# Performance work log

Measured on AMD Instinct MI355X. Metric: run time of the kernel, lower is better.

## Reference

```python
import jax, jax.numpy as jnp
import numpy as np

K_TOP = 1  # k_top in the source module


def setup_inputs() -> dict:
    key = jax.random.key(0)
    k1, k2 = jax.random.split(key)
    n_frames, dim = 8192, 1024  # n_frames_max, WavLM layer-6 feature dim
    return {
        "source_features": jax.random.normal(k1, (n_frames, dim), dtype=jnp.float32),
        "target_features": jax.random.normal(k2, (n_frames, dim), dtype=jnp.float32),
    }


def reference(source_features, target_features):
    # fast_cosine_dist: 1 - cosine_similarity, via normalized GEMM
    eps = 1e-12
    sn = source_features / jnp.maximum(
        jnp.linalg.norm(source_features, axis=-1, keepdims=True), eps)
    tn = target_features / jnp.maximum(
        jnp.linalg.norm(target_features, axis=-1, keepdims=True), eps)
    dists = 1.0 - jnp.einsum("sd,td->st", sn, tn)  # [n_src, n_tgt]
    # topk(k=K_TOP, largest=False): take top-k of negated distances
    _, idx = jax.lax.top_k(-dists, K_TOP)  # [n_src, K_TOP]
    # gather matched target frames and average over the k neighbors
    linear_target = target_features[idx].mean(axis=1)  # [n_src, dim]
    return linear_target
```

## Files before the change

### kernel.cpp

```cpp
#include <hip/hip_runtime.h>
#include <math.h>

#define DIM      1024
#define NSTRIPES 16
#define PAD      4
#define MAXSLOTS 32
#define EPS      0.08f

typedef __attribute__((ext_vector_type(8))) __bf16 bf16x8;
typedef __attribute__((ext_vector_type(4))) __bf16 bf16x4;
typedef __attribute__((ext_vector_type(4))) float f32x4;

#define FENCE() asm volatile("" ::: "memory")

__device__ __forceinline__ void async16(void* lds, const void* g) {
    __builtin_amdgcn_global_load_lds(
        (const __attribute__((address_space(1))) unsigned int*)g,
        (__attribute__((address_space(3))) unsigned int*)lds, 16, 0, 0);
}

__global__ void convertA_kernel(const float* __restrict__ in,
                                unsigned short* __restrict__ outp, int n8) {
    int i = blockIdx.x * blockDim.x + threadIdx.x;
    if (i >= n8) return;
    const float4* p = (const float4*)in;
    float4 v0 = p[2 * i], v1 = p[2 * i + 1];
    bf16x8 o;
    o[0] = (__bf16)v0.x; o[1] = (__bf16)v0.y; o[2] = (__bf16)v0.z; o[3] = (__bf16)v0.w;
    o[4] = (__bf16)v1.x; o[5] = (__bf16)v1.y; o[6] = (__bf16)v1.z; o[7] = (__bf16)v1.w;
    *(bf16x8*)(outp + (size_t)8 * i) = o;
}

__global__ void convertB_norm_kernel(const float* __restrict__ tgt,
                                     unsigned short* __restrict__ bfB,
                                     float* __restrict__ inv_t, int n) {
    int row = blockIdx.x * 4 + (threadIdx.x >> 6);
    int l = threadIdx.x & 63;
    if (row >= n) return;
    const float4* rp = (const float4*)(tgt + (size_t)row * DIM);
    unsigned short* wp = bfB + (size_t)row * DIM;
    float ss = 0.f;
#pragma unroll
    for (int p = 0; p < 4; ++p) {
        float4 v = rp[l + 64 * p];
        bf16x4 o;
        o[0] = (__bf16)v.x; o[1] = (__bf16)v.y;
        o[2] = (__bf16)v.z; o[3] = (__bf16)v.w;
        *(bf16x4*)(wp + (size_t)(l + 64 * p) * 4) = o;
        ss = fmaf(v.x, v.x, ss);
        ss = fmaf(v.y, v.y, ss);
        ss = fmaf(v.z, v.z, ss);
        ss = fmaf(v.w, v.w, ss);
    }
#pragma unroll
    for (int off = 32; off; off >>= 1) ss += __shfl_xor(ss, off, 64);
    if (l == 0) inv_t[row] = 1.0f / fmaxf(sqrtf(ss), 1e-12f);
}

__global__ __launch_bounds__(512) void mfma_argmax256_kernel(
    const unsigned short* __restrict__ Abf,
    const unsigned short* __restrict__ Bbf,
    const float* __restrict__ inv_t,
    float* __restrict__ sbest,
    int M, int N) {
    __shared__ __align__(16) unsigned short sA[2][16384];
    __shared__ __align__(16) unsigned short sB[2][16384];
    const int tid = threadIdx.x;
    const int w = tid >> 6, l = tid & 63;
    const int wr = w >> 2, wc = w & 3;
    const int rowBase = blockIdx.x * 256;
    const int colBase = blockIdx.y * 256;
    const int ngroups = N >> 3;
    const int NT = DIM / 64;

    int goff[4], lbase[4];
#pragma unroll
    for (int j = 0; j < 4; ++j) {
        int c = j * 512 + tid;
        int row = c >> 3, c8 = c & 7;
        goff[j] = row * DIM + (c8 ^ (row & 7)) * 8;
        lbase[j] = (j * 512 + w * 64) * 8;
    }

    const int q = l >> 4;
    int aoff[8], boff[4];
#pragma unroll
    for (int m = 0; m < 8; ++m) {
        int row = wr * 128 + m * 16 + (l & 15);
        aoff[m] = (row * 128 + q * 16) ^ ((row & 7) << 4);
    }
#pragma unroll
    for (int n = 0; n < 4; ++n) {
        int col = wc * 64 + n * 16 + (l & 15);
        boff[n] = (col * 128 + q * 16) ^ ((col & 7) << 4);
    }

    f32x4 acc[8][4];
#pragma unroll
    for (int m = 0; m < 8; ++m)
#pragma unroll
        for (int n = 0; n < 4; ++n) acc[m][n] = (f32x4){0.f, 0.f, 0.f, 0.f};

    const unsigned short* ga = Abf + (size_t)rowBase * DIM;
    const unsigned short* gb = Bbf + (size_t)colBase * DIM;

    auto stage = [&](int t) {
        unsigned short* dA = &sA[t & 1][0];
        unsigned short* dB = &sB[t & 1][0];
#pragma unroll
        for (int j = 0; j < 4; ++j) {
            async16(dA + lbase[j], ga + t * 64 + goff[j]);
            async16(dB + lbase[j], gb + t * 64 + goff[j]);
        }
    };
    auto compute = [&](int i) {
        const char* bA = (const char*)&sA[i & 1][0];
        const char* bB = (const char*)&sB[i & 1][0];
#pragma unroll
        for (int s = 0; s < 2; ++s) {
            bf16x8 af[8], bfr[4];
#pragma unroll
            for (int m = 0; m < 8; ++m)
                af[m] = *(const bf16x8*)(bA + (aoff[m] ^ (s << 6)));
#pragma unroll
            for (int n = 0; n < 4; ++n)
                bfr[n] = *(const bf16x8*)(bB + (boff[n] ^ (s << 6)));
            __builtin_amdgcn_s_setprio(1);
#pragma unroll
            for (int m = 0; m < 8; ++m)
#pragma unroll
                for (int n = 0; n < 4; ++n)
                    acc[m][n] = __builtin_amdgcn_mfma_f32_16x16x32_bf16(
                        bfr[n], af[m], acc[m][n], 0, 0, 0);
            __builtin_amdgcn_s_setprio(0);
        }
    };

    stage(0);
    for (int i = 0; i < NT - 1; ++i) {
        stage(i + 1);
        asm volatile("s_waitcnt vmcnt(8)" ::: "memory");
        FENCE(); __builtin_amdgcn_s_barrier(); FENCE();
        compute(i);
        FENCE(); __builtin_amdgcn_s_barrier(); FENCE();
    }
    asm volatile("s_waitcnt vmcnt(0)" ::: "memory");
    FENCE(); __builtin_amdgcn_s_barrier(); FENCE();
    compute(NT - 1);

#pragma unroll
    for (int n = 0; n < 4; ++n) {
        float4 it4 = *(const float4*)&inv_t[colBase + wc * 64 + n * 16 + (q << 2)];
#pragma unroll
        for (int m = 0; m < 8; ++m) {
            float v = acc[m][n][0] * it4.x;
            v = fmaxf(v, acc[m][n][1] * it4.y);
            v = fmaxf(v, acc[m][n][2] * it4.z);
            v = fmaxf(v, acc[m][n][3] * it4.w);
            v = fmaxf(v, __shfl_xor(v, 16, 64));
            if ((l & 16) == 0) {
                int row = rowBase + wr * 128 + m * 16 + (l & 15);
                int g = (colBase >> 3) + wc * 8 + n * 2 + (q >> 1);
                sbest[(size_t)row * ngroups + g] = v;
            }
        }
    }
}

__global__ __launch_bounds__(256) void flag_refine_kernel(
    const float* __restrict__ sbest, const float* __restrict__ src,
    const float* __restrict__ tgt, const float* __restrict__ inv_t,
    float* __restrict__ out, int ngroups, int gsh) {
    __shared__ __align__(16) float4 s_src[256];
    __shared__ float wmax[4];
    __shared__ int s_slots[MAXSLOTS];
    __shared__ int s_cnt;
    __shared__ float s_wv[4];
    __shared__ int s_wi[4];
    __shared__ int s_best;
    const int row = blockIdx.x;
    const int tid = threadIdx.x;
    const int w = tid >> 6, l = tid & 63;
    const int GW = 1 << gsh;

    s_src[tid] = ((const float4*)(src + (size_t)row * DIM))[tid];
    if (tid == 0) s_cnt = 0;

    const float* p = sbest + (size_t)row * ngroups;
    const int nper = ngroups >> 8;
    float v[4];
    float mx = -1e30f;
    for (int j = 0; j < nper; ++j) {
        v[j] = p[tid + j * 256];
        mx = fmaxf(mx, v[j]);
    }
#pragma unroll
    for (int off = 32; off; off >>= 1) mx = fmaxf(mx, __shfl_xor(mx, off, 64));
    if (l == 0) wmax[w] = mx;
    __syncthreads();
    float thr = fmaxf(fmaxf(wmax[0], wmax[1]), fmaxf(wmax[2], wmax[3])) - EPS;
    for (int j = 0; j < nper; ++j) {
        if (v[j] >= thr) {
            int s = atomicAdd(&s_cnt, 1);
            if (s < MAXSLOTS) s_slots[s] = tid + j * 256;
        }
    }
    __syncthreads();

    int m = s_cnt;
    if (m > MAXSLOTS) m = MAXSLOTS;
    const int ncand = m << gsh;
    const int grp = tid >> 4;
    const int ln = tid & 15;
    float bv = -1e30f;
    int bi = 0x7fffffff;
    for (int c = grp; c < ncand; c += 16) {
        int col = (s_slots[c >> gsh] << gsh) + (c & (GW - 1));
        const float4* trow = (const float4*)(tgt + (size_t)col * DIM);
        float dot = 0.f;
#pragma unroll
        for (int j = 0; j < 16; ++j) {
            float4 a = s_src[ln + 16 * j];
            float4 b = trow[ln + 16 * j];
            dot = fmaf(a.x, b.x, dot);
            dot = fmaf(a.y, b.y, dot);
            dot = fmaf(a.z, b.z, dot);
            dot = fmaf(a.w, b.w, dot);
        }
        dot += __shfl_xor(dot, 1, 64);
        dot += __shfl_xor(dot, 2, 64);
        dot += __shfl_xor(dot, 4, 64);
        dot += __shfl_xor(dot, 8, 64);
        float vv = dot * inv_t[col];
        if (vv > bv || (vv == bv && col < bi)) { bv = vv; bi = col; }
    }
#pragma unroll
    for (int off = 16; off <= 32; off <<= 1) {
        float v2 = __shfl_xor(bv, off, 64);
        int i2 = __shfl_xor(bi, off, 64);
        if (v2 > bv || (v2 == bv && i2 < bi)) { bv = v2; bi = i2; }
    }
    if (l == 0) { s_wv[w] = bv; s_wi[w] = bi; }
    __syncthreads();
    if (tid == 0) {
        float vv = s_wv[0];
        int ix = s_wi[0];
#pragma unroll
        for (int t = 1; t < 4; ++t) {
            float v2 = s_wv[t];
            int i2 = s_wi[t];
            if (v2 > vv || (v2 == vv && i2 < ix)) { vv = v2; ix = i2; }
        }
        s_best = ix;
    }
    __syncthreads();
    int ixb = s_best;
    ((float4*)(out + (size_t)row * DIM))[tid] =
        ((const float4*)(tgt + (size_t)ixb * DIM))[tid];
}

__global__ void inv_norm_kernel(const float* __restrict__ t,
                                float* __restrict__ inv_t, int n) {
    int wave = (int)((blockIdx.x * blockDim.x + threadIdx.x) >> 6);
    int lane = threadIdx.x & 63;
    if (wave >= n) return;
    const float4* row = (const float4*)(t + (size_t)wave * DIM);
    float ss = 0.f;
#pragma unroll
    for (int p = 0; p < 4; ++p) {
        float4 v = row[lane + 64 * p];
        ss = fmaf(v.x, v.x, ss);
        ss = fmaf(v.y, v.y, ss);
        ss = fmaf(v.z, v.z, ss);
        ss = fmaf(v.w, v.w, ss);
    }
#pragma unroll
    for (int off = 32; off; off >>= 1) ss += __shfl_xor(ss, off, 64);
    if (lane == 0) inv_t[wave] = 1.0f / fmaxf(sqrtf(ss), 1e-12f);
}

__global__ __launch_bounds__(256) void fused_argmax_kernel(
    const float* __restrict__ A, const float* __restrict__ B,
    const float* __restrict__ inv_t, float* __restrict__ sbest,
    int* __restrict__ sidx, int M, int N) {
    __shared__ __align__(16) float sA[32][128 + PAD];
    __shared__ __align__(16) float sB[32][128 + PAD];
    const int tid = threadIdx.x;
    const int tx = tid & 15;
    const int ty = tid >> 4;
    const int rowBase = blockIdx.x * 128;
    const int stripe = blockIdx.y;
    const int stripeN = N / NSTRIPES;
    const int colBase0 = stripe * stripeN;
    const int lr = tid >> 3;
    const int lk = (tid & 7) << 2;
    float best[8];
    int bidx[8];
#pragma unroll
    for (int i = 0; i < 8; ++i) { best[i] = -1e30f; bidx[i] = 0; }
    for (int nt = 0; nt < stripeN / 128; ++nt) {
        const int colBase = colBase0 + nt * 128;
        float acc[8][8];
#pragma unroll
        for (int i = 0; i < 8; ++i)
#pragma unroll
            for (int j = 0; j < 8; ++j) acc[i][j] = 0.f;
        for (int kt = 0; kt < DIM / 32; ++kt) {
            const int k0 = kt * 32;
            __syncthreads();
#pragma unroll
            for (int p = 0; p < 4; ++p) {
                int r = lr + 32 * p;
                float4 va = *(const float4*)(A + (size_t)(rowBase + r) * DIM + k0 + lk);
                sA[lk + 0][r] = va.x; sA[lk + 1][r] = va.y;
                sA[lk + 2][r] = va.z; sA[lk + 3][r] = va.w;
                float4 vb = *(const float4*)(B + (size_t)(colBase + r) * DIM + k0 + lk);
                sB[lk + 0][r] = vb.x; sB[lk + 1][r] = vb.y;
                sB[lk + 2][r] = vb.z; sB[lk + 3][r] = vb.w;
            }
            __syncthreads();
#pragma unroll 4
            for (int k = 0; k < 32; ++k) {
                float4 af0 = *(const float4*)&sA[k][ty * 8];
                float4 af1 = *(const float4*)&sA[k][ty * 8 + 4];
                float4 bf0 = *(const float4*)&sB[k][tx * 8];
                float4 bf1 = *(const float4*)&sB[k][tx * 8 + 4];
                float a[8] = {af0.x, af0.y, af0.z, af0.w, af1.x, af1.y, af1.z, af1.w};
                float b[8] = {bf0.x, bf0.y, bf0.z, bf0.w, bf1.x, bf1.y, bf1.z, bf1.w};
#pragma unroll
                for (int i = 0; i < 8; ++i)
#pragma unroll
                    for (int j = 0; j < 8; ++j)
                        acc[i][j] = fmaf(a[i], b[j], acc[i][j]);
            }
        }
#pragma unroll
        for (int j = 0; j < 8; ++j) {
            int col = colBase + tx * 8 + j;
            float it = inv_t[col];
#pragma unroll
            for (int i = 0; i < 8; ++i) {
                float s = acc[i][j] * it;
                if (s > best[i]) { best[i] = s; bidx[i] = col; }
            }
        }
    }
#pragma unroll
    for (int i = 0; i < 8; ++i) {
        float v = best[i];
        int ix = bidx[i];
#pragma unroll
        for (int off = 1; off < 16; off <<= 1) {
            float v2 = __shfl_xor(v, off, 64);
            int ix2 = __shfl_xor(ix, off, 64);
            if (v2 > v || (v2 == v && ix2 < ix)) { v = v2; ix = ix2; }
        }
        if (tx == 0) {
            int row = rowBase + ty * 8 + i;
            sbest[(size_t)stripe * M + row] = v;
            sidx[(size_t)stripe * M + row] = ix;
        }
    }
}

__global__ void gather_kernel(const float* __restrict__ B,
                              const float* __restrict__ sbest,
                              const int* __restrict__ sidx,
                              float* __restrict__ out, int M) {
    int row = blockIdx.x;
    float v = -1e30f;
    int ix = 0;
#pragma unroll
    for (int s = 0; s < NSTRIPES; ++s) {
        float v2 = sbest[(size_t)s * M + row];
        int ix2 = sidx[(size_t)s * M + row];
        if (v2 > v || (v2 == v && ix2 < ix)) { v = v2; ix = ix2; }
    }
    const float4* srcp = (const float4*)(B + (size_t)ix * DIM);
    float4* dstp = (float4*)(out + (size_t)row * DIM);
    dstp[threadIdx.x] = srcp[threadIdx.x];
}

extern "C" void kernel_launch(void* const* d_in, const int* in_sizes, int n_in,
                              void* d_out, int out_size, void* d_ws, size_t ws_size,
                              hipStream_t stream) {
    const float* src = (const float*)d_in[0];
    const float* tgt = (const float*)d_in[1];
    float* out = (float*)d_out;
    int M = in_sizes[0] / DIM;
    int N = in_sizes[1] / DIM;

    auto align256 = [](size_t x) { return (x + 255) & ~(size_t)255; };
    size_t sz_invt = align256((size_t)N * 4);
    size_t sz_bfA = align256((size_t)M * DIM * 2);
    size_t sz_bfB = align256((size_t)N * DIM * 2);
    size_t common = sz_invt + sz_bfA + sz_bfB;
    size_t sz_sbest8 = align256((size_t)M * (N / 8) * 4);

    if ((M % 256) == 0 && (N % 2048) == 0 && N / 8 <= 1024 &&
        ws_size >= common + sz_sbest8) {
        char* p = (char*)d_ws;
        float* inv_t = (float*)p;                 p += sz_invt;
        unsigned short* bfA = (unsigned short*)p; p += sz_bfA;
        unsigned short* bfB = (unsigned short*)p; p += sz_bfB;
        float* sbest = (float*)p;
        int ngroups = N >> 3;

        int n8a = M * DIM / 8;
        convertA_kernel<<<dim3((n8a + 255) / 256), 256, 0, stream>>>(src, bfA, n8a);
        convertB_norm_kernel<<<dim3((N + 3) / 4), 256, 0, stream>>>(tgt, bfB, inv_t, N);
        mfma_argmax256_kernel<<<dim3(M / 256, N / 256), 512, 0, stream>>>(
            bfA, bfB, inv_t, sbest, M, N);
        flag_refine_kernel<<<dim3(M), 256, 0, stream>>>(
            sbest, src, tgt, inv_t, out, ngroups, 3);
    } else {
        char* ws = (char*)d_ws;
        float* sbest = (float*)ws;
        int* sidx = (int*)(ws + (size_t)NSTRIPES * M * sizeof(float));
        float* inv_t = (float*)(ws + (size_t)NSTRIPES * M * (sizeof(float) + sizeof(int)));
        inv_norm_kernel<<<dim3((N + 3) / 4), 256, 0, stream>>>(tgt, inv_t, N);
        fused_argmax_kernel<<<dim3(M / 128, NSTRIPES), 256, 0, stream>>>(
            src, tgt, inv_t, sbest, sidx, M, N);
        gather_kernel<<<dim3(M), 256, 0, stream>>>(tgt, sbest, sidx, out, M);
    }
}
```

Measured before the change: 224.8 us.

## Split GEMM k-tile compute into four quadrant phases with barriers

Restructures the inner MFMA loop so each k-tile is processed in four phases, each covering a quarter of the output (half of M by half of N). Each phase loads its A and B fragments for both k-substeps, waits on LDS, and then issues 16 MFMAs between barriers and a sched_barrier. The intent is a ping-pong style interleave of LDS reads and MFMA across waves, with lower register pressure per phase. It adds many more workgroup barriers per k-tile, which may serialize waves and hurt overlap.

New measurement: 260.7 us. 1.16x slower.

```diff
diff --git a/kernel.cpp b/kernel.cpp
--- a/kernel.cpp
+++ b/kernel.cpp
@@ -113,40 +113,52 @@
             async16(dB + lbase[j], gb + t * 64 + goff[j]);
         }
     };
-    auto compute = [&](int i) {
+
+    stage(0);
+    for (int i = 0; i < NT; ++i) {
+        if (i + 1 < NT) {
+            stage(i + 1);
+            asm volatile("s_waitcnt vmcnt(8)" ::: "memory");
+        } else {
+            asm volatile("s_waitcnt vmcnt(0)" ::: "memory");
+        }
+        FENCE(); __builtin_amdgcn_s_barrier(); FENCE();
         const char* bA = (const char*)&sA[i & 1][0];
         const char* bB = (const char*)&sB[i & 1][0];
 #pragma unroll
-        for (int s = 0; s < 2; ++s) {
-            bf16x8 af[8], bfr[4];
-#pragma unroll
-            for (int m = 0; m < 8; ++m)
-                af[m] = *(const bf16x8*)(bA + (aoff[m] ^ (s << 6)));
-#pragma unroll
-            for (int n = 0; n < 4; ++n)
-                bfr[n] = *(const bf16x8*)(bB + (boff[n] ^ (s << 6)));
+        for (int ph = 0; ph < 4; ++ph) {
+            const int mh = ph >> 1, nh = ph & 1;
+            bf16x8 af[4][2], bfr[2][2];
+#pragma unroll
+            for (int mm = 0; mm < 4; ++mm)
+#pragma unroll
+                for (int ks = 0; ks < 2; ++ks)
+                    af[mm][ks] =
+                        *(const bf16x8*)(bA + (aoff[mh * 4 + mm] ^ (ks << 6)));
+#pragma unroll
+            for (int nn = 0; nn < 2; ++nn)
+#pragma unroll
+                for (int ks = 0; ks < 2; ++ks)
+                    bfr[nn][ks] =
+                        *(const bf16x8*)(bB + (boff[nh * 2 + nn] ^ (ks << 6)));
+            FENCE(); __builtin_amdgcn_s_barrier(); FENCE();
+            asm volatile("s_waitcnt lgkmcnt(0)" ::: "memory");
+            __builtin_amdgcn_sched_barrier(0);
             __builtin_amdgcn_s_setprio(1);
 #pragma unroll
-            for (int m = 0; m < 8; ++m)
-#pragma unroll
-                for (int n = 0; n < 4; ++n)
-                    acc[m][n] = __builtin_amdgcn_mfma_f32_16x16x32_bf16(
-                        bfr[n], af[m], acc[m][n], 0, 0, 0);
+            for (int ks = 0; ks < 2; ++ks)
+#pragma unroll
+                for (int mm = 0; mm < 4; ++mm)
+#pragma unroll
+                    for (int nn = 0; nn < 2; ++nn)
+                        acc[mh * 4 + mm][nh * 2 + nn] =
+                            __builtin_amdgcn_mfma_f32_16x16x32_bf16(
+                                bfr[nn][ks], af[mm][ks],
+                                acc[mh * 4 + mm][nh * 2 + nn], 0, 0, 0);
             __builtin_amdgcn_s_setprio(0);
-        }
-    };
-
-    stage(0);
-    for (int i = 0; i < NT - 1; ++i) {
-        stage(i + 1);
-        asm volatile("s_waitcnt vmcnt(8)" ::: "memory");
-        FENCE(); __builtin_amdgcn_s_barrier(); FENCE();
-        compute(i);
-        FENCE(); __builtin_amdgcn_s_barrier(); FENCE();
-    }
-    asm volatile("s_waitcnt vmcnt(0)" ::: "memory");
-    FENCE(); __builtin_amdgcn_s_barrier(); FENCE();
-    compute(NT - 1);
+            FENCE(); __builtin_amdgcn_s_barrier(); FENCE();
+        }
+    }
 
 #pragma unroll
     for (int n = 0; n < 4; ++n) {
```
